# Performance work log

Hardware: AMD Instinct MI355X
Metric: run time of the kernel (lower is better)

Reference implementation:

```python
import jax, jax.numpy as jnp
import numpy as np

NC = 6            # CPAB tessellation cells (tess_size=6, zero_boundary=True)
DIM = NC - 1      # theta dimension = 5
SIG_LEN = 2048
CHANNELS = 3
BATCH = 256
FC_IN = 64 * 168  # flattened net_part1 output for signal_len=2048
NUM_SCALING = 0   # N in transform_data_ss
EPS_BN = 1e-5


def _cpab_basis():
    """QR null-space basis of the CPAB continuity + zero-boundary constraints.
    Params ordered [a_1,b_1,...,a_NC,b_NC]; v(x)=a_c x + b_c on cell c."""
    nc = NC
    L = np.zeros((nc + 1, 2 * nc))
    for k in range(1, nc):  # continuity at internal knots x_k = k/nc
        xk = k / nc
        L[k - 1, 2 * (k - 1)] = xk
        L[k - 1, 2 * (k - 1) + 1] = 1.0
        L[k - 1, 2 * k] = -xk
        L[k - 1, 2 * k + 1] = -1.0
    L[nc - 1, 1] = 1.0        # v(0) = 0  -> b_1 = 0
    L[nc, 2 * (nc - 1)] = 1.0  # v(1) = 0 -> a_nc + b_nc = 0
    L[nc, 2 * nc - 1] = 1.0
    Q, _ = np.linalg.qr(L.T, mode='complete')
    return np.ascontiguousarray(Q[:, nc + 1:]).astype(np.float32)  # (12, 5)


def _conv1d(x, w, b):
    y = jax.lax.conv_general_dilated(x, w, (1,), 'VALID',
                                     dimension_numbers=('NCH', 'OIH', 'NCH'))
    return y + b[None, :, None]


def _maxpool1d(x, k, s):
    return jax.lax.reduce_window(x, -jnp.inf, jax.lax.max, (1, 1, k), (1, 1, s), 'VALID')


def _bn(x, g, b, m, v):  # eval-mode BatchNorm1d
    return (x - m[None, :, None]) * (g / jnp.sqrt(v + EPS_BN))[None, :, None] + b[None, :, None]


def _integrate(x, A):
    """Exact CPAB 1D flow integration over t=1 with cell-crossing handling.
    x: (B, n) points in [0,1]; A: (B, NC, 2) per-cell (a, b). Monotone
    trajectories cross at most NC-1 boundaries -> fixed NC+1 iterations."""
    a_all, b_all = A[:, :, 0], A[:, :, 1]
    t = jnp.ones_like(x)
    for _ in range(NC + 1):
        c = jnp.clip(jnp.floor(x * NC).astype(jnp.int32), 0, NC - 1)
        a = jnp.take_along_axis(a_all, c, axis=1)
        b = jnp.take_along_axis(b_all, c, axis=1)
        v = a * x + b
        xb = jnp.where(v >= 0, (c + 1).astype(x.dtype) / NC, c.astype(x.dtype) / NC)
        big_a = jnp.abs(a) > 1e-8
        a_s = jnp.where(big_a, a, 1.0)
        z = x + b / a_s        # shifted coord: x(t) = z*exp(a t) - b/a
        zb = xb + b / a_s
        ratio = zb / jnp.where(jnp.abs(z) > 1e-12, z, 1e-12)
        t_exp = jnp.log(jnp.maximum(ratio, 1e-12)) / a_s
        v_s = jnp.where(jnp.abs(v) > 1e-12, v, 1.0)
        t_lin = (xb - x) / v_s
        thit = jnp.where(big_a, t_exp, t_lin)
        valid = (jnp.abs(v) > 1e-12) & (thit > 0) & (jnp.where(big_a, ratio, 1.0) > 0)
        thit = jnp.where(valid, thit, jnp.inf)
        tau = jnp.minimum(t, thit)
        x_new = jnp.where(big_a, z * jnp.exp(a * tau) - (z - x), x + b * tau)
        hit = thit <= t
        nudge = jnp.where(v >= 0, 1e-6, -1e-6)  # push into next cell
        x = jnp.clip(jnp.where(hit, xb + nudge, x_new), 0.0, 1.0)
        t = jnp.maximum(t - tau, 0.0)
    return x


def _interp1d(data, pos):
    """data: (B, L, C); pos: (B, n) in [0,1] -> (B, n, C) linear interpolation."""
    Lw = data.shape[1]
    p = jnp.clip(pos, 0.0, 1.0) * (Lw - 1)
    x0 = jnp.clip(jnp.floor(p).astype(jnp.int32), 0, Lw - 2)
    w = (p - x0.astype(p.dtype))[:, :, None]
    d0 = jnp.take_along_axis(data, x0[:, :, None], axis=1)
    d1 = jnp.take_along_axis(data, (x0 + 1)[:, :, None], axis=1)
    return d0 * (1.0 - w) + d1 * w


def _transform_data_ss(data, theta, basis, outsize, N):
    """CPAB scaling-and-squaring warp of data (B, L, C) by theta (B, DIM)."""
    Bsz = theta.shape[0]
    A = (theta @ basis.T).reshape(Bsz, NC, 2) / (2.0 ** N)
    grid = jnp.linspace(0.0, 1.0, outsize, dtype=data.dtype)
    grid_t = _integrate(jnp.broadcast_to(grid, (Bsz, outsize)), A)
    for _ in range(N):  # squaring: compose the warp with itself
        grid_t = _interp1d(grid_t[:, :, None], grid_t)[:, :, 0]
    return _interp1d(data, grid_t)


def reference(x, conv1_w, conv1_b, bn1_g, bn1_b, bn1_m, bn1_v,
              conv2_w, conv2_b, bn2_g, bn2_b, bn2_m, bn2_v,
              conv3_w, conv3_b, bn3_g, bn3_b, bn3_m, bn3_v,
              fc1_w, fc1_b, fc2_w, fc2_b, fc3_w, fc3_b, fc4_w, fc4_b, basis):
    # localization net (n_recurrence = 1, back_version = True)
    h = jax.nn.relu(_maxpool1d(_bn(_conv1d(x, conv1_w, conv1_b), bn1_g, bn1_b, bn1_m, bn1_v), 3, 2))
    h = jax.nn.relu(_maxpool1d(_bn(_conv1d(h, conv2_w, conv2_b), bn2_g, bn2_b, bn2_m, bn2_v), 3, 3))
    h = jax.nn.relu(_maxpool1d(_bn(_conv1d(h, conv3_w, conv3_b), bn3_g, bn3_b, bn3_m, bn3_v), 3, 2))
    xs = h.reshape(h.shape[0], -1)  # (B, 64*168)
    xs = jax.nn.relu(xs @ fc1_w.T + fc1_b)
    xs = jax.nn.relu(xs @ fc2_w.T + fc2_b)
    xs = jax.nn.relu(xs @ fc3_w.T + fc3_b)
    theta = jnp.tanh(xs @ fc4_w.T + fc4_b)  # (B, 5)
    data = jnp.transpose(x, (0, 2, 1))       # (B, L, C)
    warped = _transform_data_ss(data, theta, basis, SIG_LEN, NUM_SCALING)
    return jnp.transpose(warped, (0, 2, 1))  # (B, C, L)


def setup_inputs() -> dict:
    key = jax.random.key(0)
    ks = jax.random.split(key, 16)
    def nrm(k, shape, scale):
        return (jax.random.normal(k, shape) * scale).astype(jnp.float32)
    inp = {}
    inp['x'] = jax.random.normal(ks[0], (BATCH, CHANNELS, SIG_LEN), dtype=jnp.float32)
    inp['conv1_w'] = nrm(ks[1], (128, CHANNELS, 3), (CHANNELS * 3) ** -0.5)
    inp['conv1_b'] = nrm(ks[2], (128,), 0.01)
    inp['bn1_g'] = jnp.ones((128,), jnp.float32)
    inp['bn1_b'] = jnp.zeros((128,), jnp.float32)
    inp['bn1_m'] = nrm(ks[3], (128,), 0.1)
    inp['bn1_v'] = jnp.ones((128,), jnp.float32)
    inp['conv2_w'] = nrm(ks[4], (64, 128, 5), (128 * 5) ** -0.5)
    inp['conv2_b'] = nrm(ks[5], (64,), 0.01)
    inp['bn2_g'] = jnp.ones((64,), jnp.float32)
    inp['bn2_b'] = jnp.zeros((64,), jnp.float32)
    inp['bn2_m'] = nrm(ks[6], (64,), 0.1)
    inp['bn2_v'] = jnp.ones((64,), jnp.float32)
    inp['conv3_w'] = nrm(ks[7], (64, 64, 3), (64 * 3) ** -0.5)
    inp['conv3_b'] = nrm(ks[8], (64,), 0.01)
    inp['bn3_g'] = jnp.ones((64,), jnp.float32)
    inp['bn3_b'] = jnp.zeros((64,), jnp.float32)
    inp['bn3_m'] = nrm(ks[9], (64,), 0.1)
    inp['bn3_v'] = jnp.ones((64,), jnp.float32)
    inp['fc1_w'] = nrm(ks[10], (48, FC_IN), FC_IN ** -0.5)
    inp['fc1_b'] = jnp.zeros((48,), jnp.float32)
    inp['fc2_w'] = nrm(ks[11], (32, 48), 48 ** -0.5)
    inp['fc2_b'] = jnp.zeros((32,), jnp.float32)
    inp['fc3_w'] = nrm(ks[12], (16, 32), 32 ** -0.5)
    inp['fc3_b'] = jnp.zeros((16,), jnp.float32)
    # near-identity warp head (original zero-inits weight, identity bias)
    inp['fc4_w'] = nrm(ks[13], (DIM, 16), 0.01)
    inp['fc4_b'] = nrm(ks[14], (DIM,), 0.01)
    inp['basis'] = jnp.asarray(_cpab_basis())
    return inp
```

## Files before the change

### kernel.cpp

```cpp
#include <hip/hip_runtime.h>
#include <math.h>

#define BATCH   256
#define SIGLEN  2048
#define L1OUT   1022
#define L2OUT   339
#define L3OUT   168
#define FCIN    10752

#define TP2   21
#define NROW  68
#define H1S   136

#define TU3   28

typedef float f32x4 __attribute__((ext_vector_type(4)));
typedef short s16x8 __attribute__((ext_vector_type(8)));

__device__ __forceinline__ unsigned short f2bf(float f) {
    unsigned int u = __float_as_uint(f);
    return (unsigned short)((u + 0x7fffu + ((u >> 16) & 1u)) >> 16);
}
__device__ __forceinline__ float bf2f(unsigned short h) {
    return __uint_as_float(((unsigned int)h) << 16);
}

__launch_bounds__(256)
__global__ void prep_kernel(
    const float* __restrict__ conv1_b,
    const float* __restrict__ g1, const float* __restrict__ b1,
    const float* __restrict__ m1, const float* __restrict__ v1,
    const float* __restrict__ conv2_w, const float* __restrict__ conv2_b,
    const float* __restrict__ g2, const float* __restrict__ b2,
    const float* __restrict__ m2, const float* __restrict__ v2,
    const float* __restrict__ conv3_w, const float* __restrict__ conv3_b,
    const float* __restrict__ g3, const float* __restrict__ b3,
    const float* __restrict__ m3, const float* __restrict__ v3,
    const float* __restrict__ fc1_w,
    unsigned short* __restrict__ w2hi, unsigned short* __restrict__ w2lo,
    unsigned short* __restrict__ w3hi, unsigned short* __restrict__ w3lo,
    float* __restrict__ wp1,
    float* __restrict__ so1, float* __restrict__ so2, float* __restrict__ so3)
{
    int tid = blockIdx.x * 256 + threadIdx.x;
    int stride = gridDim.x * 256;
    for (int i = tid; i < 64*128*5; i += stride) {
        int co = i / 640; int rr = i - co*640; int ci = rr / 5; int k = rr - ci*5;
        float w = conv2_w[i];
        unsigned short hi = f2bf(w);
        unsigned short lo = f2bf(w - bf2f(hi));
        int dst = ((k*4 + (ci >> 5))*64 + co)*32 + (ci & 31);
        w2hi[dst] = hi;
        w2lo[dst] = lo;
    }
    for (int i = tid; i < 64*64*3; i += stride) {
        int co = i / 192; int r = i - co*192; int ci = r / 3; int k = r - ci*3;
        float w = conv3_w[i];
        unsigned short hi = f2bf(w);
        unsigned short lo = f2bf(w - bf2f(hi));
        int dst = ((k*2 + (ci >> 5))*64 + co)*32 + (ci & 31);
        w3hi[dst] = hi;
        w3lo[dst] = lo;
    }
    for (int i = tid; i < 48*FCIN; i += stride) {
        int o = i / FCIN; int ph = i - o*FCIN;
        int u = ph >> 6, co = ph & 63;
        wp1[i] = fc1_w[o*FCIN + co*L3OUT + u];
    }
    if (tid < 128) {
        float s = g1[tid] / sqrtf(v1[tid] + 1e-5f);
        so1[tid]       = s;
        so1[128 + tid] = (conv1_b[tid] - m1[tid]) * s + b1[tid];
    }
    if (tid < 64) {
        float s2 = g2[tid] / sqrtf(v2[tid] + 1e-5f);
        so2[tid]      = s2;
        so2[64 + tid] = (conv2_b[tid] - m2[tid]) * s2 + b2[tid];
        float s3 = g3[tid] / sqrtf(v3[tid] + 1e-5f);
        so3[tid]      = s3;
        so3[64 + tid] = (conv3_b[tid] - m3[tid]) * s3 + b3[tid];
    }
}

__launch_bounds__(256, 4)
__global__ void conv12_kernel(
    const float* __restrict__ x, const float* __restrict__ w1,
    const unsigned short* __restrict__ w2hi, const unsigned short* __restrict__ w2lo,
    const float* __restrict__ so1, const float* __restrict__ so2,
    unsigned int* __restrict__ h2p)
{
    __shared__ unsigned short h1hi[NROW * H1S];
    __shared__ unsigned short h1lo[NROW * H1S];

    int t  = threadIdx.x;
    int b  = blockIdx.x;
    int u0 = blockIdx.y * TP2;
    int q0 = 3 * u0;
    int wv = __builtin_amdgcn_readfirstlane(t >> 6);
    int l  = t & 63;
    int m  = l & 15;
    int qd = l >> 4;
    int cp = wv & 1;
    int pp = wv >> 1;

    float wr[2][9];
    float s1r[2], o1r[2];
    #pragma unroll
    for (int h = 0; h < 2; ++h) {
        int ch = l + 64*h;
        #pragma unroll
        for (int j = 0; j < 9; ++j) wr[h][j] = w1[ch*9 + j];
        s1r[h] = so1[ch]; o1r[h] = so1[128 + ch];
    }
    for (int s = 0; s < 17; ++s) {
        int r = 4*s + wv;
        int xbase = 2*(q0 + r);
        float xv[3][5];
        #pragma unroll
        for (int ci = 0; ci < 3; ++ci) {
            const float* xp = x + (b*3 + ci)*SIGLEN;
            #pragma unroll
            for (int d = 0; d < 5; ++d) {
                int xi = xbase + d; xi = xi < SIGLEN ? xi : SIGLEN - 1;
                xv[ci][d] = xp[xi];
            }
        }
        #pragma unroll
        for (int h = 0; h < 2; ++h) {
            float r0 = 0.f, r1 = 0.f, r2 = 0.f;
            #pragma unroll
            for (int ci = 0; ci < 3; ++ci) {
                float wA = wr[h][ci*3], wB = wr[h][ci*3+1], wC = wr[h][ci*3+2];
                r0 = fmaf(xv[ci][0], wA, fmaf(xv[ci][1], wB, fmaf(xv[ci][2], wC, r0)));
                r1 = fmaf(xv[ci][1], wA, fmaf(xv[ci][2], wB, fmaf(xv[ci][3], wC, r1)));
                r2 = fmaf(xv[ci][2], wA, fmaf(xv[ci][3], wB, fmaf(xv[ci][4], wC, r2)));
            }
            float mx = fmaxf(r0, fmaxf(r1, r2));
            float v  = fmaxf(fmaf(s1r[h], mx, o1r[h]), 0.f);
            unsigned short hi = f2bf(v);
            unsigned short lo = f2bf(v - bf2f(hi));
            h1hi[r*H1S + l + 64*h] = hi;
            h1lo[r*H1S + l + 64*h] = lo;
        }
    }
    __syncthreads();

    f32x4 acc[2][2] = {{(f32x4)(0.f), (f32x4)(0.f)}, {(f32x4)(0.f), (f32x4)(0.f)}};

    const unsigned short* whb0 = w2hi + (2*cp  )*512 + m*32 + qd*8;
    const unsigned short* whb1 = w2hi + (2*cp+1)*512 + m*32 + qd*8;
    const unsigned short* wlb0 = w2lo + (2*cp  )*512 + m*32 + qd*8;
    const unsigned short* wlb1 = w2lo + (2*cp+1)*512 + m*32 + qd*8;

    for (int k = 0; k < 5; ++k) {
        #pragma unroll
        for (int cb = 0; cb < 4; ++cb) {
            int st = k*4 + cb;
            s16x8 wh0 = *(const s16x8*)(whb0 + st*2048);
            s16x8 wl0 = *(const s16x8*)(wlb0 + st*2048);
            s16x8 wh1 = *(const s16x8*)(whb1 + st*2048);
            s16x8 wl1 = *(const s16x8*)(wlb1 + st*2048);
            #pragma unroll
            for (int ptl = 0; ptl < 2; ++ptl) {
                int row = (2*pp + ptl)*16 + m + k;
                s16x8 ah = *(const s16x8*)&h1hi[row*H1S + cb*32 + qd*8];
                s16x8 al = *(const s16x8*)&h1lo[row*H1S + cb*32 + qd*8];
                acc[0][ptl] = __builtin_amdgcn_mfma_f32_16x16x32_bf16(ah, wh0, acc[0][ptl], 0, 0, 0);
                acc[0][ptl] = __builtin_amdgcn_mfma_f32_16x16x32_bf16(al, wh0, acc[0][ptl], 0, 0, 0);
                acc[0][ptl] = __builtin_amdgcn_mfma_f32_16x16x32_bf16(ah, wl0, acc[0][ptl], 0, 0, 0);
                acc[1][ptl] = __builtin_amdgcn_mfma_f32_16x16x32_bf16(ah, wh1, acc[1][ptl], 0, 0, 0);
                acc[1][ptl] = __builtin_amdgcn_mfma_f32_16x16x32_bf16(al, wh1, acc[1][ptl], 0, 0, 0);
                acc[1][ptl] = __builtin_amdgcn_mfma_f32_16x16x32_bf16(ah, wl1, acc[1][ptl], 0, 0, 0);
            }
        }
    }
    __syncthreads();

    float* c2 = (float*)h1hi;
    #pragma unroll
    for (int ctl = 0; ctl < 2; ++ctl)
        #pragma unroll
        for (int ptl = 0; ptl < 2; ++ptl)
            #pragma unroll
            for (int rg = 0; rg < 4; ++rg)
                c2[((2*pp + ptl)*16 + qd*4 + rg)*65 + (2*cp + ctl)*16 + m] = acc[ctl][ptl][rg];
    __syncthreads();

    #pragma unroll
    for (int it = 0; it < 6; ++it) {
        int idx = t + it*256;
        if (idx < TP2*64) {
            int ul = idx >> 6, co = idx & 63;
            int u = u0 + ul;
            if (u < L2OUT) {
                float v0 = c2[(3*ul  )*65 + co];
                float v1 = c2[(3*ul+1)*65 + co];
                float v2 = c2[(3*ul+2)*65 + co];
                float mm = fmaxf(v0, fmaxf(v1, v2));
                float v  = fmaxf(fmaf(so2[co], mm, so2[64 + co]), 0.f);
                unsigned short hi = f2bf(v);
                unsigned short lo = f2bf(v - bf2f(hi));
                h2p[(b*L2OUT + u)*64 + co] = (unsigned int)hi | ((unsigned int)lo << 16);
            }
        }
    }
}

__launch_bounds__(256, 4)
__global__ void conv3_kernel(
    const unsigned int* __restrict__ h2p,
    const unsigned short* __restrict__ w3hi, const unsigned short* __restrict__ w3lo,
    const float* __restrict__ so3, float* __restrict__ xs)
{
    __shared__ unsigned short h3hi[66 * 72];
    __shared__ unsigned short h3lo[66 * 72];

    int t  = threadIdx.x;
    int b  = blockIdx.x;
    int u0 = blockIdx.y * TU3;
    int wv = __builtin_amdgcn_readfirstlane(t >> 6);
    int l  = t & 63;
    int m  = l & 15;
    int qd = l >> 4;

    for (int i = t; i < 66*64; i += 256) {
        int r = i >> 6, ci = i & 63;
        int g = 2*u0 + r; g = g > (L2OUT-1) ? (L2OUT-1) : g;
        unsigned int v = h2p[(b*L2OUT + g)*64 + ci];
        h3hi[r*72 + ci] = (unsigned short)(v & 0xffffu);
        h3lo[r*72 + ci] = (unsigned short)(v >> 16);
    }
    __syncthreads();

    s16x8 wh[6], wl[6];
    #pragma unroll
    for (int s = 0; s < 6; ++s) {
        wh[s] = *(const s16x8*)(w3hi + s*2048 + (wv*16 + m)*32 + qd*8);
        wl[s] = *(const s16x8*)(w3lo + s*2048 + (wv*16 + m)*32 + qd*8);
    }

    f32x4 acc[4] = {(f32x4)(0.f), (f32x4)(0.f), (f32x4)(0.f), (f32x4)(0.f)};
    #pragma unroll
    for (int pt = 0; pt < 4; ++pt) {
        #pragma unroll
        for (int s = 0; s < 6; ++s) {
            int row = pt*16 + m + (s >> 1);
            int off = (s & 1)*32 + qd*8;
            s16x8 ah = *(const s16x8*)&h3hi[row*72 + off];
            s16x8 al = *(const s16x8*)&h3lo[row*72 + off];
            acc[pt] = __builtin_amdgcn_mfma_f32_16x16x32_bf16(ah, wh[s], acc[pt], 0, 0, 0);
            acc[pt] = __builtin_amdgcn_mfma_f32_16x16x32_bf16(al, wh[s], acc[pt], 0, 0, 0);
            acc[pt] = __builtin_amdgcn_mfma_f32_16x16x32_bf16(ah, wl[s], acc[pt], 0, 0, 0);
        }
    }
    __syncthreads();

    float* c3 = (float*)h3hi;
    #pragma unroll
    for (int pt = 0; pt < 4; ++pt)
        #pragma unroll
        for (int rg = 0; rg < 4; ++rg)
            c3[(pt*16 + qd*4 + rg)*65 + wv*16 + m] = acc[pt][rg];
    __syncthreads();

    #pragma unroll
    for (int it = 0; it < 7; ++it) {
        int idx = t + it*256;
        if (idx < TU3*64) {
            int ul = idx >> 6, co = idx & 63;
            int p = 2*ul;
            float v0 = c3[(p  )*65 + co];
            float v1 = c3[(p+1)*65 + co];
            float v2 = c3[(p+2)*65 + co];
            float mm = fmaxf(v0, fmaxf(v1, v2));
            xs[b*FCIN + (u0 + ul)*64 + co] = fmaxf(fmaf(so3[co], mm, so3[64 + co]), 0.f);
        }
    }
}

__launch_bounds__(256)
__global__ void fc1_kernel(
    const float* __restrict__ xs, const float* __restrict__ w,
    float* __restrict__ part)
{
    int t = threadIdx.x, lane = t & 63, wid = t >> 6;
    int b0 = blockIdx.x * 4;
    int kc = blockIdx.y;
    int o0 = wid * 12;
    float acc[48];
    #pragma unroll
    for (int i = 0; i < 48; ++i) acc[i] = 0.f;

    int kbase = kc * 1344 + lane;
    for (int ki = 0; ki < 21; ++ki) {
        int k = kbase + ki * 64;
        float xv0 = xs[(b0 + 0) * FCIN + k];
        float xv1 = xs[(b0 + 1) * FCIN + k];
        float xv2 = xs[(b0 + 2) * FCIN + k];
        float xv3 = xs[(b0 + 3) * FCIN + k];
        #pragma unroll
        for (int j = 0; j < 12; ++j) {
            float ww = w[(o0 + j) * FCIN + k];
            acc[j]      += xv0 * ww;
            acc[12 + j] += xv1 * ww;
            acc[24 + j] += xv2 * ww;
            acc[36 + j] += xv3 * ww;
        }
    }
    #pragma unroll
    for (int i = 0; i < 48; ++i) {
        #pragma unroll
        for (int off = 32; off > 0; off >>= 1)
            acc[i] += __shfl_xor(acc[i], off, 64);
    }
    if (lane == 0) {
        #pragma unroll
        for (int bb = 0; bb < 4; ++bb)
            #pragma unroll
            for (int j = 0; j < 12; ++j)
                part[((b0 + bb) * 48 + o0 + j) * 8 + kc] = acc[bb * 12 + j];
    }
}

__launch_bounds__(256)
__global__ void fc234_kernel(
    const float* __restrict__ part, const float* __restrict__ fc1_b,
    const float* __restrict__ fc2_w, const float* __restrict__ fc2_b,
    const float* __restrict__ fc3_w, const float* __restrict__ fc3_b,
    const float* __restrict__ fc4_w, const float* __restrict__ fc4_b,
    const float* __restrict__ basis, float* __restrict__ A)
{
    __shared__ float xsl[256 * 49];
    __shared__ float w2l[1536], w3l[512], w4l[80];
    __shared__ float b2l[32], b3l[16], b4l[8], basl[60];
    int t = threadIdx.x;
    for (int i = t; i < 256 * 48; i += 256) {
        const float4* p = (const float4*)&part[i * 8];
        float4 pa = p[0], pb = p[1];
        float sv = ((pa.x + pa.y) + (pa.z + pa.w)) + ((pb.x + pb.y) + (pb.z + pb.w));
        xsl[(i / 48) * 49 + (i % 48)] = fmaxf(sv + fc1_b[i % 48], 0.f);
    }
    for (int i = t; i < 1536; i += 256) w2l[i] = fc2_w[i];
    for (int i = t; i < 512;  i += 256) w3l[i] = fc3_w[i];
    if (t < 80) w4l[t] = fc4_w[t];
    if (t < 32) b2l[t] = fc2_b[t];
    if (t < 16) b3l[t] = fc3_b[t];
    if (t < 5)  b4l[t] = fc4_b[t];
    if (t < 60) basl[t] = basis[t];
    __syncthreads();

    const float* xin = &xsl[t * 49];
    float h[32];
    #pragma unroll 4
    for (int o = 0; o < 32; ++o) {
        float sv = b2l[o];
        for (int i = 0; i < 48; ++i) sv += w2l[o * 48 + i] * xin[i];
        h[o] = fmaxf(sv, 0.f);
    }
    float g[16];
    #pragma unroll 4
    for (int o = 0; o < 16; ++o) {
        float sv = b3l[o];
        for (int i = 0; i < 32; ++i) sv += w3l[o * 32 + i] * h[i];
        g[o] = fmaxf(sv, 0.f);
    }
    float th[5];
    #pragma unroll
    for (int o = 0; o < 5; ++o) {
        float sv = b4l[o];
        for (int i = 0; i < 16; ++i) sv += w4l[o * 16 + i] * g[i];
        th[o] = tanhf(sv);
    }
    #pragma unroll
    for (int j = 0; j < 12; ++j) {
        float sv = 0.f;
        #pragma unroll
        for (int d = 0; d < 5; ++d) sv += basl[j * 5 + d] * th[d];
        A[t * 12 + j] = sv;
    }
}

__launch_bounds__(256)
__global__ void warp_kernel(
    const float* __restrict__ x, const float* __restrict__ A,
    float* __restrict__ out)
{
    __shared__ float Al[12];
    int b = blockIdx.x;
    int i = blockIdx.y * 256 + threadIdx.x;
    if (threadIdx.x < 12) Al[threadIdx.x] = A[b * 12 + threadIdx.x];
    __syncthreads();

    float xp = (float)i / 2047.f;
    float t  = 1.f;
    for (int it = 0; it < 7; ++it) {
        int c = (int)floorf(xp * 6.f);
        c = min(max(c, 0), 5);
        float a  = Al[2 * c], bb = Al[2 * c + 1];
        float v  = a * xp + bb;
        float xb = (v >= 0.f) ? (float)(c + 1) / 6.f : (float)c / 6.f;
        bool  big_a = fabsf(a) > 1e-8f;
        float a_s = big_a ? a : 1.f;
        float z   = xp + bb / a_s;
        float zb  = xb + bb / a_s;
        float zden = (fabsf(z) > 1e-12f) ? z : 1e-12f;
        float ratio = zb / zden;
        float t_exp = logf(fmaxf(ratio, 1e-12f)) / a_s;
        float v_s   = (fabsf(v) > 1e-12f) ? v : 1.f;
        float t_lin = (xb - xp) / v_s;
        float thit  = big_a ? t_exp : t_lin;
        bool valid  = (fabsf(v) > 1e-12f) && (thit > 0.f) && ((big_a ? ratio : 1.f) > 0.f);
        if (!valid) thit = __builtin_inff();
        float tau   = fminf(t, thit);
        float x_new = big_a ? (z * expf(a * tau) - (z - xp)) : (xp + bb * tau);
        bool hit    = (thit <= t);
        float nudge = (v >= 0.f) ? 1e-6f : -1e-6f;
        xp = hit ? (xb + nudge) : x_new;
        xp = fminf(fmaxf(xp, 0.f), 1.f);
        t  = fmaxf(t - tau, 0.f);
    }
    float p = fminf(fmaxf(xp, 0.f), 1.f) * 2047.f;
    int i0 = (int)floorf(p);
    i0 = min(max(i0, 0), 2046);
    float w = p - (float)i0;
    #pragma unroll
    for (int c = 0; c < 3; ++c) {
        const float* d = &x[(b * 3 + c) * SIGLEN];
        out[(b * 3 + c) * SIGLEN + i] = d[i0] * (1.f - w) + d[i0 + 1] * w;
    }
}

extern "C" void kernel_launch(void* const* d_in, const int* in_sizes, int n_in,
                              void* d_out, int out_size, void* d_ws, size_t ws_size,
                              hipStream_t stream) {
    (void)in_sizes; (void)n_in; (void)out_size; (void)ws_size;
    const float* x       = (const float*)d_in[0];
    const float* conv1_w = (const float*)d_in[1];
    const float* conv1_b = (const float*)d_in[2];
    const float* bn1_g   = (const float*)d_in[3];
    const float* bn1_b   = (const float*)d_in[4];
    const float* bn1_m   = (const float*)d_in[5];
    const float* bn1_v   = (const float*)d_in[6];
    const float* conv2_w = (const float*)d_in[7];
    const float* conv2_b = (const float*)d_in[8];
    const float* bn2_g   = (const float*)d_in[9];
    const float* bn2_b   = (const float*)d_in[10];
    const float* bn2_m   = (const float*)d_in[11];
    const float* bn2_v   = (const float*)d_in[12];
    const float* conv3_w = (const float*)d_in[13];
    const float* conv3_b = (const float*)d_in[14];
    const float* bn3_g   = (const float*)d_in[15];
    const float* bn3_b   = (const float*)d_in[16];
    const float* bn3_m   = (const float*)d_in[17];
    const float* bn3_v   = (const float*)d_in[18];
    const float* fc1_w   = (const float*)d_in[19];
    const float* fc1_b   = (const float*)d_in[20];
    const float* fc2_w   = (const float*)d_in[21];
    const float* fc2_b   = (const float*)d_in[22];
    const float* fc3_w   = (const float*)d_in[23];
    const float* fc3_b   = (const float*)d_in[24];
    const float* fc4_w   = (const float*)d_in[25];
    const float* fc4_b   = (const float*)d_in[26];
    const float* basis   = (const float*)d_in[27];

    unsigned short* w2hi = (unsigned short*)d_ws;
    unsigned short* w2lo = w2hi + 40960;
    unsigned short* w3hi = w2lo + 40960;
    unsigned short* w3lo = w3hi + 12288;
    float* ws   = (float*)d_ws;
    float* so1  = ws + 53248;
    float* so2  = so1 + 256;
    float* so3  = so2 + 128;
    float* wp1  = so3 + 128;
    unsigned int* h2p = (unsigned int*)(wp1 + 516096);
    float* xs   = wp1 + 516096 + 5554176;
    float* part = xs  + 2752512;
    float* Aws  = part + 98304;

    prep_kernel<<<256, 256, 0, stream>>>(
        conv1_b, bn1_g, bn1_b, bn1_m, bn1_v,
        conv2_w, conv2_b, bn2_g, bn2_b, bn2_m, bn2_v,
        conv3_w, conv3_b, bn3_g, bn3_b, bn3_m, bn3_v,
        fc1_w, w2hi, w2lo, w3hi, w3lo, wp1, so1, so2, so3);

    dim3 g2(BATCH, (L2OUT + TP2 - 1) / TP2);
    conv12_kernel<<<g2, 256, 0, stream>>>(x, conv1_w, w2hi, w2lo, so1, so2, h2p);

    dim3 g3(BATCH, L3OUT / TU3);
    conv3_kernel<<<g3, 256, 0, stream>>>(h2p, w3hi, w3lo, so3, xs);

    dim3 gfc(BATCH / 4, 8);
    fc1_kernel<<<gfc, 256, 0, stream>>>(xs, wp1, part);

    fc234_kernel<<<1, 256, 0, stream>>>(part, fc1_b, fc2_w, fc2_b, fc3_w, fc3_b,
                                        fc4_w, fc4_b, basis, Aws);

    dim3 g5(BATCH, SIGLEN / 256);
    warp_kernel<<<g5, 256, 0, stream>>>(x, Aws, (float*)d_out);
}
```

Baseline: 287.3 us.

## Process two batches per conv12 block, split fc1 K into 12 chunks, coalesce weight repack

conv12 now handles two batch samples per block, so each conv2 weight fragment loaded from global memory feeds twice as many MFMAs. The block's LDS doubles and the occupancy hint drops to 2. The fc1 reduction is split into 12 K-chunks instead of 8 for more parallelism, and fc234 sums 12 partials. The fc1 weight repack now reads the source contiguously and scatters the writes. Together these raise register and LDS pressure in conv12 in exchange for fewer weight loads and more fc1 blocks.

```diff
diff --git a/kernel.cpp b/kernel.cpp
--- a/kernel.cpp
+++ b/kernel.cpp
@@ -11,8 +11,12 @@
 #define TP2   21
 #define NROW  68
 #define H1S   136
+#define H1SZ  (NROW*H1S)
 
 #define TU3   28
+
+#define KC1   12
+#define KCL   (FCIN/KC1)
 
 typedef float f32x4 __attribute__((ext_vector_type(4)));
 typedef short s16x8 __attribute__((ext_vector_type(8)));
@@ -63,9 +67,9 @@
         w3lo[dst] = lo;
     }
     for (int i = tid; i < 48*FCIN; i += stride) {
-        int o = i / FCIN; int ph = i - o*FCIN;
-        int u = ph >> 6, co = ph & 63;
-        wp1[i] = fc1_w[o*FCIN + co*L3OUT + u];
+        int o = i / FCIN; int r = i - o*FCIN;
+        int co = r / L3OUT, u = r - co*L3OUT;
+        wp1[o*FCIN + u*64 + co] = fc1_w[i];
     }
     if (tid < 128) {
         float s = g1[tid] / sqrtf(v1[tid] + 1e-5f);
@@ -82,18 +86,18 @@
     }
 }
 
-__launch_bounds__(256, 4)
+__launch_bounds__(256, 2)
 __global__ void conv12_kernel(
     const float* __restrict__ x, const float* __restrict__ w1,
     const unsigned short* __restrict__ w2hi, const unsigned short* __restrict__ w2lo,
     const float* __restrict__ so1, const float* __restrict__ so2,
     unsigned int* __restrict__ h2p)
 {
-    __shared__ unsigned short h1hi[NROW * H1S];
-    __shared__ unsigned short h1lo[NROW * H1S];
+    __shared__ unsigned short h1hi[2 * H1SZ];
+    __shared__ unsigned short h1lo[2 * H1SZ];
 
     int t  = threadIdx.x;
-    int b  = blockIdx.x;
+    int b0 = blockIdx.x * 2;
     int u0 = blockIdx.y * TP2;
     int q0 = 3 * u0;
     int wv = __builtin_amdgcn_readfirstlane(t >> 6);
@@ -112,40 +116,49 @@
         for (int j = 0; j < 9; ++j) wr[h][j] = w1[ch*9 + j];
         s1r[h] = so1[ch]; o1r[h] = so1[128 + ch];
     }
-    for (int s = 0; s < 17; ++s) {
-        int r = 4*s + wv;
-        int xbase = 2*(q0 + r);
-        float xv[3][5];
-        #pragma unroll
-        for (int ci = 0; ci < 3; ++ci) {
-            const float* xp = x + (b*3 + ci)*SIGLEN;
+    for (int bb = 0; bb < 2; ++bb) {
+        const float* xb = x + (b0 + bb)*3*SIGLEN;
+        for (int s = 0; s < 17; ++s) {
+            int r = 4*s + wv;
+            int xbase = 2*(q0 + r);
+            float xv[3][5];
             #pragma unroll
-            for (int d = 0; d < 5; ++d) {
-                int xi = xbase + d; xi = xi < SIGLEN ? xi : SIGLEN - 1;
-                xv[ci][d] = xp[xi];
+            for (int ci = 0; ci < 3; ++ci) {
+                const float* xp = xb + ci*SIGLEN;
+                #pragma unroll
+                for (int d = 0; d < 5; ++d) {
+                    int xi = xbase + d; xi = xi < SIGLEN ? xi : SIGLEN - 1;
+                    xv[ci][d] = xp[xi];
+                }
+            }
+            #pragma unroll
+            for (int h = 0; h < 2; ++h) {
+                float r0 = 0.f, r1 = 0.f, r2 = 0.f;
+                #pragma unroll
+                for (int ci = 0; ci < 3; ++ci) {
+                    float wA = wr[h][ci*3], wB = wr[h][ci*3+1], wC = wr[h][ci*3+2];
+                    r0 = fmaf(xv[ci][0], wA, fmaf(xv[ci][1], wB, fmaf(xv[ci][2], wC, r0)));
+                    r1 = fmaf(xv[ci][1], wA, fmaf(xv[ci][2], wB, fmaf(xv[ci][3], wC, r1)));
+                    r2 = fmaf(xv[ci][2], wA, fmaf(xv[ci][3], wB, fmaf(xv[ci][4], wC, r2)));
+                }
+                float mx = fmaxf(r0, fmaxf(r1, r2));
+                float v  = fmaxf(fmaf(s1r[h], mx, o1r[h]), 0.f);
+                unsigned short hi = f2bf(v);
+                unsigned short lo = f2bf(v - bf2f(hi));
+                h1hi[bb*H1SZ + r*H1S + l + 64*h] = hi;
+                h1lo[bb*H1SZ + r*H1S + l + 64*h] = lo;
             }
         }
-        #pragma unroll
-        for (int h = 0; h < 2; ++h) {
-            float r0 = 0.f, r1 = 0.f, r2 = 0.f;
+    }
+    __syncthreads();
+
+    f32x4 acc[2][2][2];
+    #pragma unroll
+    for (int bb = 0; bb < 2; ++bb)
+        #pragma unroll
+        for (int c = 0; c < 2; ++c)
             #pragma unroll
-            for (int ci = 0; ci < 3; ++ci) {
-                float wA = wr[h][ci*3], wB = wr[h][ci*3+1], wC = wr[h][ci*3+2];
-                r0 = fmaf(xv[ci][0], wA, fmaf(xv[ci][1], wB, fmaf(xv[ci][2], wC, r0)));
-                r1 = fmaf(xv[ci][1], wA, fmaf(xv[ci][2], wB, fmaf(xv[ci][3], wC, r1)));
-                r2 = fmaf(xv[ci][2], wA, fmaf(xv[ci][3], wB, fmaf(xv[ci][4], wC, r2)));
-            }
-            float mx = fmaxf(r0, fmaxf(r1, r2));
-            float v  = fmaxf(fmaf(s1r[h], mx, o1r[h]), 0.f);
-            unsigned short hi = f2bf(v);
-            unsigned short lo = f2bf(v - bf2f(hi));
-            h1hi[r*H1S + l + 64*h] = hi;
-            h1lo[r*H1S + l + 64*h] = lo;
-        }
-    }
-    __syncthreads();
-
-    f32x4 acc[2][2] = {{(f32x4)(0.f), (f32x4)(0.f)}, {(f32x4)(0.f), (f32x4)(0.f)}};
+            for (int p = 0; p < 2; ++p) acc[bb][c][p] = (f32x4)(0.f);
 
     const unsigned short* whb0 = w2hi + (2*cp  )*512 + m*32 + qd*8;
     const unsigned short* whb1 = w2hi + (2*cp+1)*512 + m*32 + qd*8;
@@ -161,16 +174,19 @@
             s16x8 wh1 = *(const s16x8*)(whb1 + st*2048);
             s16x8 wl1 = *(const s16x8*)(wlb1 + st*2048);
             #pragma unroll
-            for (int ptl = 0; ptl < 2; ++ptl) {
-                int row = (2*pp + ptl)*16 + m + k;
-                s16x8 ah = *(const s16x8*)&h1hi[row*H1S + cb*32 + qd*8];
-                s16x8 al = *(const s16x8*)&h1lo[row*H1S + cb*32 + qd*8];
-                acc[0][ptl] = __builtin_amdgcn_mfma_f32_16x16x32_bf16(ah, wh0, acc[0][ptl], 0, 0, 0);
-                acc[0][ptl] = __builtin_amdgcn_mfma_f32_16x16x32_bf16(al, wh0, acc[0][ptl], 0, 0, 0);
-                acc[0][ptl] = __builtin_amdgcn_mfma_f32_16x16x32_bf16(ah, wl0, acc[0][ptl], 0, 0, 0);
-                acc[1][ptl] = __builtin_amdgcn_mfma_f32_16x16x32_bf16(ah, wh1, acc[1][ptl], 0, 0, 0);
-                acc[1][ptl] = __builtin_amdgcn_mfma_f32_16x16x32_bf16(al, wh1, acc[1][ptl], 0, 0, 0);
-                acc[1][ptl] = __builtin_amdgcn_mfma_f32_16x16x32_bf16(ah, wl1, acc[1][ptl], 0, 0, 0);
+            for (int bb = 0; bb < 2; ++bb) {
+                #pragma unroll
+                for (int ptl = 0; ptl < 2; ++ptl) {
+                    int row = (2*pp + ptl)*16 + m + k;
+                    s16x8 ah = *(const s16x8*)&h1hi[bb*H1SZ + row*H1S + cb*32 + qd*8];
+                    s16x8 al = *(const s16x8*)&h1lo[bb*H1SZ + row*H1S + cb*32 + qd*8];
+                    acc[bb][0][ptl] = __builtin_amdgcn_mfma_f32_16x16x32_bf16(ah, wh0, acc[bb][0][ptl], 0, 0, 0);
+                    acc[bb][0][ptl] = __builtin_amdgcn_mfma_f32_16x16x32_bf16(al, wh0, acc[bb][0][ptl], 0, 0, 0);
+                    acc[bb][0][ptl] = __builtin_amdgcn_mfma_f32_16x16x32_bf16(ah, wl0, acc[bb][0][ptl], 0, 0, 0);
+                    acc[bb][1][ptl] = __builtin_amdgcn_mfma_f32_16x16x32_bf16(ah, wh1, acc[bb][1][ptl], 0, 0, 0);
+                    acc[bb][1][ptl] = __builtin_amdgcn_mfma_f32_16x16x32_bf16(al, wh1, acc[bb][1][ptl], 0, 0, 0);
+                    acc[bb][1][ptl] = __builtin_amdgcn_mfma_f32_16x16x32_bf16(ah, wl1, acc[bb][1][ptl], 0, 0, 0);
+                }
             }
         }
     }
@@ -178,29 +194,34 @@
 
     float* c2 = (float*)h1hi;
     #pragma unroll
-    for (int ctl = 0; ctl < 2; ++ctl)
-        #pragma unroll
-        for (int ptl = 0; ptl < 2; ++ptl)
+    for (int bb = 0; bb < 2; ++bb)
+        #pragma unroll
+        for (int ctl = 0; ctl < 2; ++ctl)
             #pragma unroll
-            for (int rg = 0; rg < 4; ++rg)
-                c2[((2*pp + ptl)*16 + qd*4 + rg)*65 + (2*cp + ctl)*16 + m] = acc[ctl][ptl][rg];
-    __syncthreads();
-
-    #pragma unroll
-    for (int it = 0; it < 6; ++it) {
+            for (int ptl = 0; ptl < 2; ++ptl)
+                #pragma unroll
+                for (int rg = 0; rg < 4; ++rg)
+                    c2[bb*4160 + ((2*pp + ptl)*16 + qd*4 + rg)*65 + (2*cp + ctl)*16 + m] = acc[bb][ctl][ptl][rg];
+    __syncthreads();
+
+    #pragma unroll
+    for (int it = 0; it < 11; ++it) {
         int idx = t + it*256;
-        if (idx < TP2*64) {
-            int ul = idx >> 6, co = idx & 63;
+        if (idx < 2*TP2*64) {
+            int bb = idx / (TP2*64);
+            int r  = idx - bb*(TP2*64);
+            int ul = r >> 6, co = r & 63;
             int u = u0 + ul;
             if (u < L2OUT) {
-                float v0 = c2[(3*ul  )*65 + co];
-                float v1 = c2[(3*ul+1)*65 + co];
-                float v2 = c2[(3*ul+2)*65 + co];
+                const float* cc = c2 + bb*4160;
+                float v0 = cc[(3*ul  )*65 + co];
+                float v1 = cc[(3*ul+1)*65 + co];
+                float v2 = cc[(3*ul+2)*65 + co];
                 float mm = fmaxf(v0, fmaxf(v1, v2));
                 float v  = fmaxf(fmaf(so2[co], mm, so2[64 + co]), 0.f);
                 unsigned short hi = f2bf(v);
                 unsigned short lo = f2bf(v - bf2f(hi));
-                h2p[(b*L2OUT + u)*64 + co] = (unsigned int)hi | ((unsigned int)lo << 16);
+                h2p[((b0 + bb)*L2OUT + u)*64 + co] = (unsigned int)hi | ((unsigned int)lo << 16);
             }
         }
     }
@@ -291,8 +312,8 @@
     #pragma unroll
     for (int i = 0; i < 48; ++i) acc[i] = 0.f;
 
-    int kbase = kc * 1344 + lane;
-    for (int ki = 0; ki < 21; ++ki) {
+    int kbase = kc * KCL + lane;
+    for (int ki = 0; ki < KCL/64; ++ki) {
         int k = kbase + ki * 64;
         float xv0 = xs[(b0 + 0) * FCIN + k];
         float xv1 = xs[(b0 + 1) * FCIN + k];
@@ -318,7 +339,7 @@
         for (int bb = 0; bb < 4; ++bb)
             #pragma unroll
             for (int j = 0; j < 12; ++j)
-                part[((b0 + bb) * 48 + o0 + j) * 8 + kc] = acc[bb * 12 + j];
+                part[((b0 + bb) * 48 + o0 + j) * KC1 + kc] = acc[bb * 12 + j];
     }
 }
 
@@ -335,9 +356,11 @@
     __shared__ float b2l[32], b3l[16], b4l[8], basl[60];
     int t = threadIdx.x;
     for (int i = t; i < 256 * 48; i += 256) {
-        const float4* p = (const float4*)&part[i * 8];
-        float4 pa = p[0], pb = p[1];
-        float sv = ((pa.x + pa.y) + (pa.z + pa.w)) + ((pb.x + pb.y) + (pb.z + pb.w));
+        const float4* p = (const float4*)&part[i * KC1];
+        float4 pa = p[0], pb = p[1], pc = p[2];
+        float sv = ((pa.x + pa.y) + (pa.z + pa.w))
+                 + ((pb.x + pb.y) + (pb.z + pb.w))
+                 + ((pc.x + pc.y) + (pc.z + pc.w));
         xsl[(i / 48) * 49 + (i % 48)] = fmaxf(sv + fc1_b[i % 48], 0.f);
     }
     for (int i = t; i < 1536; i += 256) w2l[i] = fc2_w[i];
@@ -475,7 +498,7 @@
     unsigned int* h2p = (unsigned int*)(wp1 + 516096);
     float* xs   = wp1 + 516096 + 5554176;
     float* part = xs  + 2752512;
-    float* Aws  = part + 98304;
+    float* Aws  = part + 147456;
 
     prep_kernel<<<256, 256, 0, stream>>>(
         conv1_b, bn1_g, bn1_b, bn1_m, bn1_v,
@@ -483,13 +506,13 @@
         conv3_w, conv3_b, bn3_g, bn3_b, bn3_m, bn3_v,
         fc1_w, w2hi, w2lo, w3hi, w3lo, wp1, so1, so2, so3);
 
-    dim3 g2(BATCH, (L2OUT + TP2 - 1) / TP2);
+    dim3 g2(BATCH/2, (L2OUT + TP2 - 1) / TP2);
     conv12_kernel<<<g2, 256, 0, stream>>>(x, conv1_w, w2hi, w2lo, so1, so2, h2p);
 
     dim3 g3(BATCH, L3OUT / TU3);
     conv3_kernel<<<g3, 256, 0, stream>>>(h2p, w3hi, w3lo, so3, xs);
 
-    dim3 gfc(BATCH / 4, 8);
+    dim3 gfc(BATCH / 4, KC1);
     fc1_kernel<<<gfc, 256, 0, stream>>>(xs, wp1, part);
 
     fc234_kernel<<<1, 256, 0, stream>>>(part, fc1_b, fc2_w, fc2_b, fc3_w, fc3_b,
```

New measurement: 317.4 us. +10.5%, slower.
